# Performance work log

Hardware: AMD Instinct MI355X
Metric: run time of the kernel (lower is better)

The kernel has to match this reference:

```python
import jax, jax.numpy as jnp
import numpy as np

EPS = 1e-6

def _complex_log(x):
    # real = log(clamp_min(|x|, eps)); imag = pi where x < 0 else 0
    real = jnp.log(jnp.maximum(jnp.abs(x), EPS))
    imag = jnp.where(x < 0, np.float32(np.pi), np.float32(0.0))
    return jax.lax.complex(real, imag)

def _clogaddexp(a, b):
    # stable log(exp(a)+exp(b)) for complex a, b (shift by max of real parts)
    m = jnp.maximum(a.real, b.real)
    return jnp.log(jnp.exp(a - m) + jnp.exp(b - m)) + m

def _min_gru(h, g):
    # log-space minGRU linear recurrence over the last axis
    log_coeffs = -jax.nn.softplus(g)                      # [..., L] real
    log_values = _complex_log(h) - jax.nn.softplus(-g)    # [..., L] complex
    a_star = jnp.cumsum(log_coeffs, axis=-1)              # [..., L] real
    z = log_values - a_star                               # complex
    log_h0_plus_b_star = jax.lax.associative_scan(_clogaddexp, z, axis=-1)
    log_h = a_star + log_h0_plus_b_star
    return jnp.exp(log_h).real

def _min_gru_bidirectional(x):
    # x: [B, H, L] with H divisible by 4
    H = x.shape[1]
    fore, back = x[:, : H // 2], x[:, H // 2 :]
    fh, fg = fore[:, : H // 4], fore[:, H // 4 :]
    back = jnp.flip(back, axis=2)  # matches torch .flip(2) for [B,H,L]
    bh, bg = back[:, : H // 4], back[:, H // 4 :]
    out_f = _min_gru(fh, fg)
    out_b = jnp.flip(_min_gru(bh, bg), axis=2)
    return jnp.concatenate([out_f, out_b], axis=1)  # [B, H/2, L]

def setup_inputs() -> dict:
    key = jax.random.key(0)
    x = jax.random.normal(key, (16, 512, 4096), dtype=jnp.float32)
    return {"x": x}

def reference(x):
    return _min_gru_bidirectional(x)
```

## Files before the change

### kernel.cpp

```cpp
#include <hip/hip_runtime.h>


#define T_LEN 4096
#define CHUNK 16
#define NTHR 256

__global__ __launch_bounds__(NTHR) void mingru_bidir_kernel(
    const float* __restrict__ x, float* __restrict__ out) {
  const int row = blockIdx.x;
  const int b   = row >> 8;
  const int c   = row & 255;
  const int tid = threadIdx.x;
  const bool bwd = (c >= 128);
  const int j = c & 127;

  const float* __restrict__ hptr =
      x + ((size_t)b * 512 + (bwd ? 256 : 0) + j) * T_LEN;
  const float* __restrict__ gptr =
      x + ((size_t)b * 512 + (bwd ? 384 : 128) + j) * T_LEN;
  float* __restrict__ optr = out + ((size_t)b * 256 + c) * T_LEN;

  const int t0 = bwd ? (T_LEN - CHUNK - (tid << 4)) : (tid << 4);

  float cc[CHUNK], vv[CHUNK];

  #pragma unroll
  for (int q = 0; q < 4; ++q) {
    const float4 h4 = *reinterpret_cast<const float4*>(hptr + t0 + 4 * q);
    const float4 g4 = *reinterpret_cast<const float4*>(gptr + t0 + 4 * q);
    const float hs[4] = {h4.x, h4.y, h4.z, h4.w};
    const float gs[4] = {g4.x, g4.y, g4.z, g4.w};
    #pragma unroll
    for (int r = 0; r < 4; ++r) {
      const int e = 4 * q + r;
      const float h = hs[r];
      const float g = gs[r];
      const float ah = fmaxf(fabsf(h), 1e-6f);
      const float hp = (h < 0.0f) ? -ah : ah;
      const float eg  = __expf(-fabsf(g));
      const float inv = 1.0f / (1.0f + eg);
      const float sg  = (g >= 0.0f) ? inv : eg * inv;
      const float co  = (g >= 0.0f) ? eg * inv : inv;
      cc[e] = co;
      vv[e] = sg * hp;
    }
  }

  if (bwd) {
    #pragma unroll
    for (int e = 0; e < CHUNK / 2; ++e) {
      float t1 = cc[e]; cc[e] = cc[CHUNK - 1 - e]; cc[CHUNK - 1 - e] = t1;
      float t2 = vv[e]; vv[e] = vv[CHUNK - 1 - e]; vv[CHUNK - 1 - e] = t2;
    }
  }

  float C = cc[0], V = vv[0];
  #pragma unroll
  for (int e = 1; e < CHUNK; ++e) {
    V = cc[e] * V + vv[e];
    C = C * cc[e];
  }

  __shared__ float sC[NTHR], sV[NTHR];
  sC[tid] = C; sV[tid] = V;
  __syncthreads();
  #pragma unroll
  for (int off = 1; off < NTHR; off <<= 1) {
    float pc = 1.0f, pv = 0.0f;
    if (tid >= off) { pc = sC[tid - off]; pv = sV[tid - off]; }
    __syncthreads();
    if (tid >= off) {
      V = C * pv + V;
      C = C * pc;
      sC[tid] = C; sV[tid] = V;
    }
    __syncthreads();
  }
  const float incoming = (tid == 0) ? 0.0f : sV[tid - 1];

  float st = incoming;
  #pragma unroll
  for (int e = 0; e < CHUNK; ++e) {
    st = cc[e] * st + vv[e];
    vv[e] = st;
  }

  if (bwd) {
    #pragma unroll
    for (int e = 0; e < CHUNK / 2; ++e) {
      float t2 = vv[e]; vv[e] = vv[CHUNK - 1 - e]; vv[CHUNK - 1 - e] = t2;
    }
  }

  #pragma unroll
  for (int q = 0; q < 4; ++q) {
    *reinterpret_cast<float4*>(optr + t0 + 4 * q) =
        make_float4(vv[4 * q], vv[4 * q + 1], vv[4 * q + 2], vv[4 * q + 3]);
  }
}

extern "C" void kernel_launch(void* const* d_in, const int* in_sizes, int n_in,
                              void* d_out, int out_size, void* d_ws, size_t ws_size,
                              hipStream_t stream) {
  const float* x = (const float*)d_in[0];
  float* out = (float*)d_out;
  const int rows = 16 * 256;
  mingru_bidir_kernel<<<rows, NTHR, 0, stream>>>(x, out);
}
```

Baseline: 41.72 us.

## Replace shared-memory block scan with wavefront shuffle scan and nontemporal IO

Replaces the 8-step block-wide Hillis-Steele scan, which used shared memory and two barriers per step, with a 64-lane shuffle scan inside each wavefront. The four wavefront totals are then combined through a single barrier. Global loads and stores become nontemporal, and the gate math uses the hardware reciprocal and 1-sg for the coefficient. This removes most barrier and LDS traffic in exchange for slightly less accurate rcp and 1-sg arithmetic.

```diff
diff --git a/kernel.cpp b/kernel.cpp
--- a/kernel.cpp
+++ b/kernel.cpp
@@ -5,12 +5,16 @@
 #define CHUNK 16
 #define NTHR 256
 
+typedef float f32x4 __attribute__((ext_vector_type(4)));
+
 __global__ __launch_bounds__(NTHR) void mingru_bidir_kernel(
     const float* __restrict__ x, float* __restrict__ out) {
   const int row = blockIdx.x;
   const int b   = row >> 8;
   const int c   = row & 255;
   const int tid = threadIdx.x;
+  const int lane = tid & 63;
+  const int wid  = tid >> 6;
   const bool bwd = (c >= 128);
   const int j = c & 127;
 
@@ -26,22 +30,21 @@
 
   #pragma unroll
   for (int q = 0; q < 4; ++q) {
-    const float4 h4 = *reinterpret_cast<const float4*>(hptr + t0 + 4 * q);
-    const float4 g4 = *reinterpret_cast<const float4*>(gptr + t0 + 4 * q);
-    const float hs[4] = {h4.x, h4.y, h4.z, h4.w};
-    const float gs[4] = {g4.x, g4.y, g4.z, g4.w};
+    const f32x4 h4 =
+        __builtin_nontemporal_load(reinterpret_cast<const f32x4*>(hptr + t0 + 4 * q));
+    const f32x4 g4 =
+        __builtin_nontemporal_load(reinterpret_cast<const f32x4*>(gptr + t0 + 4 * q));
     #pragma unroll
     for (int r = 0; r < 4; ++r) {
       const int e = 4 * q + r;
-      const float h = hs[r];
-      const float g = gs[r];
+      const float h = h4[r];
+      const float g = g4[r];
       const float ah = fmaxf(fabsf(h), 1e-6f);
       const float hp = (h < 0.0f) ? -ah : ah;
       const float eg  = __expf(-fabsf(g));
-      const float inv = 1.0f / (1.0f + eg);
+      const float inv = __builtin_amdgcn_rcpf(1.0f + eg);
       const float sg  = (g >= 0.0f) ? inv : eg * inv;
-      const float co  = (g >= 0.0f) ? eg * inv : inv;
-      cc[e] = co;
+      cc[e] = 1.0f - sg;
       vv[e] = sg * hp;
     }
   }
@@ -61,22 +64,25 @@
     C = C * cc[e];
   }
 
-  __shared__ float sC[NTHR], sV[NTHR];
-  sC[tid] = C; sV[tid] = V;
-  __syncthreads();
   #pragma unroll
-  for (int off = 1; off < NTHR; off <<= 1) {
-    float pc = 1.0f, pv = 0.0f;
-    if (tid >= off) { pc = sC[tid - off]; pv = sV[tid - off]; }
-    __syncthreads();
-    if (tid >= off) {
+  for (int off = 1; off < 64; off <<= 1) {
+    const float pc = __shfl_up(C, off);
+    const float pv = __shfl_up(V, off);
+    if (lane >= off) {
       V = C * pv + V;
       C = C * pc;
-      sC[tid] = C; sV[tid] = V;
     }
-    __syncthreads();
   }
-  const float incoming = (tid == 0) ? 0.0f : sV[tid - 1];
+
+  __shared__ float sC[4], sV[4];
+  if (lane == 63) { sC[wid] = C; sV[wid] = V; }
+  __syncthreads();
+  float acc = 0.0f;
+  for (int w = 0; w < wid; ++w) acc = sC[w] * acc + sV[w];
+
+  const float pC = __shfl_up(C, 1);
+  const float pV = __shfl_up(V, 1);
+  const float incoming = (lane == 0) ? acc : pC * acc + pV;
 
   float st = incoming;
   #pragma unroll
@@ -94,8 +100,8 @@
 
   #pragma unroll
   for (int q = 0; q < 4; ++q) {
-    *reinterpret_cast<float4*>(optr + t0 + 4 * q) =
-        make_float4(vv[4 * q], vv[4 * q + 1], vv[4 * q + 2], vv[4 * q + 3]);
+    const f32x4 o4 = {vv[4 * q], vv[4 * q + 1], vv[4 * q + 2], vv[4 * q + 3]};
+    __builtin_nontemporal_store(o4, reinterpret_cast<f32x4*>(optr + t0 + 4 * q));
   }
 }
 
```

Result: slower. 71.57 us (+71.6%).
